# Kernel tuning notes

Measured on AMD Instinct MI355X. Metric: run time of the kernel, lower is better.

## Reference

```python
import jax, jax.numpy as jnp
import numpy as np

K_NN = 32
LN_EPS = 1e-5
P_JOINT = 0.95      # safety_priorities['structural_joints']
P_PLATFORM = 0.9    # safety_priorities['working_platforms']


def _sqdist(a, b):
    # a:[B,M,3], b:[B,N,3] -> [B,M,N] squared euclidean distances
    return jnp.maximum(jnp.sum(a * a, -1)[:, :, None] + jnp.sum(b * b, -1)[:, None, :]
                       - 2.0 * jnp.einsum('bmd,bnd->bmn', a, b), 0.0)


def _gather(arr, idx):
    # arr:[B,N,D], idx:[B,C] -> [B,C,D]
    B, C = idx.shape
    return jnp.take_along_axis(arr, jnp.broadcast_to(idx[:, :, None], (B, C, arr.shape[-1])), axis=1)


def _fps(coords, num_samples):
    # iterative farthest point sampling (deterministic start at index 0)
    B, N, _ = coords.shape
    start = jnp.zeros((B,), jnp.int32)
    dist0 = jnp.full((B, N), jnp.inf, coords.dtype)
    samp0 = jnp.zeros((B, num_samples), jnp.int32)

    def body(i, carry):
        dist, samp, last = carry
        last_pts = _gather(coords, last[:, None])                 # [B,1,3]
        d = jnp.sqrt(jnp.sum((coords - last_pts) ** 2, -1))       # [B,N]
        dist = jnp.minimum(dist, d)
        nxt = jnp.argmax(dist, 1).astype(jnp.int32)
        dist = dist.at[jnp.arange(B), nxt].set(0.0)
        samp = samp.at[:, i].set(nxt)
        return dist, samp, nxt

    _, samp, _ = jax.lax.fori_loop(1, num_samples, body, (dist0, samp0, start))
    return samp


def _safety(coords, scale):
    # per-point safety score [B,N], computed on the full point cloud (as in original)
    N = coords.shape[1]
    z = coords[:, :, 2]
    if scale == 'global':
        return 1.0 + jax.nn.sigmoid((z - z.mean(1, keepdims=True)) / 5.0) * P_JOINT
    if scale == 'component':
        zv = jnp.var(z, axis=1, keepdims=True, ddof=1)            # torch.var is unbiased
        return jnp.broadcast_to(1.0 + jnp.exp(-zv / 0.1) * P_PLATFORM, z.shape)
    # detail: full NxN cdist -> connection density (dist < 0.5  <=>  sqdist < 0.25)
    d2 = _sqdist(coords, coords)                                  # [B,N,N]
    density = jnp.sum(d2 < 0.25, -1).astype(coords.dtype)
    return 1.0 + density / N * P_JOINT


def _select_scale(features, coords, C, S, W1, b1, W2, b2, scale):
    idx = _fps(coords, C)                     # [B,C]
    cfeat = _gather(features, idx)            # [B,C,D]
    ccoord = _gather(coords, idx)             # [B,C,3]
    # kNN max-pooled local features (computed by original module; not used downstream)
    knn_d2 = _sqdist(ccoord, coords)          # [B,C,N]
    _, knn = jax.lax.top_k(-knn_d2, K_NN)
    _local = jax.vmap(lambda f, i: f[i])(features, knn).max(2)    # [B,C,D]
    # per-center safety score: per-point score gathered at FPS centers
    safety = jnp.take_along_axis(_safety(coords, scale), idx, axis=1)  # [B,C]
    # selector MLP: Linear -> ReLU -> Linear -> Sigmoid
    probs = jax.nn.sigmoid(jnp.maximum(cfeat @ W1.T + b1, 0.0) @ W2.T + b2)  # [B,C,S]
    final = probs.mean(-1) * safety           # [B,C] per-center score
    _, top = jax.lax.top_k(final, S)          # [B,S]
    return _gather(cfeat, top)                # [B,S,D]


def _forward(pf, pc, g_W1, g_b1, g_W2, g_b2, c_W1, c_b1, c_W2, c_b2,
             d_W1, d_b1, d_W2, d_b2, p_W1, p_b1, p_W2, p_b2, ln_g, ln_b):
    g = _select_scale(pf, pc, 256, 16, g_W1, g_b1, g_W2, g_b2, 'global')
    c = _select_scale(pf, pc, 128, 16, c_W1, c_b1, c_W2, c_b2, 'component')
    d = _select_scale(pf, pc, 64, 8, d_W1, d_b1, d_W2, d_b2, 'detail')
    toks = jnp.concatenate([g, c, d], 1)      # [B,40,D]
    # prompt_mlp: Linear(D,D/2) -> ReLU -> Linear(D/2,D) -> LayerNorm(D)
    h = jnp.maximum(toks @ p_W1.T + p_b1, 0.0) @ p_W2.T + p_b2
    mu = h.mean(-1, keepdims=True)
    var = h.var(-1, keepdims=True)
    return (h - mu) * jax.lax.rsqrt(var + LN_EPS) * ln_g + ln_b


def setup_inputs() -> dict:
    key = jax.random.key(0)
    B, N, D = 2, 8192, 768
    ks = iter(jax.random.split(key, 32))

    def nrm(shape, s=0.02):
        return jax.random.normal(next(ks), shape, jnp.float32) * s

    inp = {
        'point_features': jax.random.normal(next(ks), (B, N, D), jnp.float32),
        'point_coords': jax.random.normal(next(ks), (B, N, 3), jnp.float32) * 2.0,
    }
    for p, C, S in [('g', 256, 16), ('c', 128, 16), ('d', 64, 8)]:
        inp[p + '_W1'] = nrm((C, D)); inp[p + '_b1'] = jnp.zeros((C,), jnp.float32)
        inp[p + '_W2'] = nrm((S, C)); inp[p + '_b2'] = jnp.zeros((S,), jnp.float32)
    inp['p_W1'] = nrm((D // 2, D)); inp['p_b1'] = jnp.zeros((D // 2,), jnp.float32)
    inp['p_W2'] = nrm((D, D // 2)); inp['p_b2'] = jnp.zeros((D,), jnp.float32)
    inp['ln_g'] = jnp.ones((D,), jnp.float32); inp['ln_b'] = jnp.zeros((D,), jnp.float32)
    return inp


def reference(point_features, point_coords, g_W1, g_b1, g_W2, g_b2,
              c_W1, c_b1, c_W2, c_b2, d_W1, d_b1, d_W2, d_b2,
              p_W1, p_b1, p_W2, p_b2, ln_g, ln_b):
    return _forward(point_features, point_coords, g_W1, g_b1, g_W2, g_b2,
                    c_W1, c_b1, c_W2, c_b2, d_W1, d_b1, d_W2, d_b2,
                    p_W1, p_b1, p_W2, p_b2, ln_g, ln_b)
```

## Files before the change

### kernel.cpp

```cpp
#include <hip/hip_runtime.h>
#include <math.h>

#define N_PTS 8192
#define D_FEAT 768

typedef float v2f __attribute__((ext_vector_type(2)));

__device__ __forceinline__ float wred_max_f32(float x) {
    int v = __float_as_int(x), o;
    o = __builtin_amdgcn_update_dpp(0, v, 0x111, 0xf, 0xf, false); v = __float_as_int(fmaxf(__int_as_float(v), __int_as_float(o)));
    o = __builtin_amdgcn_update_dpp(0, v, 0x112, 0xf, 0xf, false); v = __float_as_int(fmaxf(__int_as_float(v), __int_as_float(o)));
    o = __builtin_amdgcn_update_dpp(0, v, 0x114, 0xf, 0xf, false); v = __float_as_int(fmaxf(__int_as_float(v), __int_as_float(o)));
    o = __builtin_amdgcn_update_dpp(0, v, 0x118, 0xf, 0xf, false); v = __float_as_int(fmaxf(__int_as_float(v), __int_as_float(o)));
    o = __builtin_amdgcn_update_dpp(0, v, 0x142, 0xa, 0xf, false); v = __float_as_int(fmaxf(__int_as_float(v), __int_as_float(o)));
    o = __builtin_amdgcn_update_dpp(0, v, 0x143, 0xc, 0xf, false); v = __float_as_int(fmaxf(__int_as_float(v), __int_as_float(o)));
    return __int_as_float(__builtin_amdgcn_readlane(v, 63));
}
__device__ __forceinline__ int wred_min_i32(int x) {
    int v = x, o;
    o = __builtin_amdgcn_update_dpp(0x7fffffff, v, 0x111, 0xf, 0xf, false); v = (o < v) ? o : v;
    o = __builtin_amdgcn_update_dpp(0x7fffffff, v, 0x112, 0xf, 0xf, false); v = (o < v) ? o : v;
    o = __builtin_amdgcn_update_dpp(0x7fffffff, v, 0x114, 0xf, 0xf, false); v = (o < v) ? o : v;
    o = __builtin_amdgcn_update_dpp(0x7fffffff, v, 0x118, 0xf, 0xf, false); v = (o < v) ? o : v;
    o = __builtin_amdgcn_update_dpp(0x7fffffff, v, 0x142, 0xa, 0xf, false); v = (o < v) ? o : v;
    o = __builtin_amdgcn_update_dpp(0x7fffffff, v, 0x143, 0xc, 0xf, false); v = (o < v) ? o : v;
    return __builtin_amdgcn_readlane(v, 63);
}
__device__ __forceinline__ float wred_add_f32(float x) {
    int v = __float_as_int(x), o;
    o = __builtin_amdgcn_update_dpp(0, v, 0x111, 0xf, 0xf, false); v = __float_as_int(__int_as_float(v) + __int_as_float(o));
    o = __builtin_amdgcn_update_dpp(0, v, 0x112, 0xf, 0xf, false); v = __float_as_int(__int_as_float(v) + __int_as_float(o));
    o = __builtin_amdgcn_update_dpp(0, v, 0x114, 0xf, 0xf, false); v = __float_as_int(__int_as_float(v) + __int_as_float(o));
    o = __builtin_amdgcn_update_dpp(0, v, 0x118, 0xf, 0xf, false); v = __float_as_int(__int_as_float(v) + __int_as_float(o));
    o = __builtin_amdgcn_update_dpp(0, v, 0x142, 0xa, 0xf, false); v = __float_as_int(__int_as_float(v) + __int_as_float(o));
    o = __builtin_amdgcn_update_dpp(0, v, 0x143, 0xc, 0xf, false); v = __float_as_int(__int_as_float(v) + __int_as_float(o));
    return __int_as_float(__builtin_amdgcn_readlane(v, 63));
}

#define DPP64_STEP(cur, ctrl, rmask)                                                        \
    {                                                                                       \
        unsigned _h = (unsigned)__builtin_amdgcn_update_dpp(0, (int)(unsigned)((cur) >> 32), ctrl, rmask, 0xf, false); \
        unsigned _l = (unsigned)__builtin_amdgcn_update_dpp(0, (int)(unsigned)(cur), ctrl, rmask, 0xf, false);         \
        unsigned long long _o = ((unsigned long long)_h << 32) | _l;                        \
        cur = (_o > (cur)) ? _o : (cur);                                                    \
    }

__global__ __launch_bounds__(512, 2) __attribute__((amdgpu_waves_per_eu(2)))
void fps_kernel(const float* __restrict__ coords,
                int* __restrict__ idx_all,
                float* __restrict__ safety_all) {
#pragma clang fp contract(off)
    const int b = blockIdx.x;
    const int t = threadIdx.x;
    const float* cb = coords + (size_t)b * N_PTS * 3;

    v2f px2[8], py2[8], pz2[8], m2p[8];
#pragma unroll
    for (int j = 0; j < 8; j++) {
        int p0 = t + (2 * j) * 512, p1 = t + (2 * j + 1) * 512;
        px2[j].x = cb[p0 * 3 + 0]; px2[j].y = cb[p1 * 3 + 0];
        py2[j].x = cb[p0 * 3 + 1]; py2[j].y = cb[p1 * 3 + 1];
        pz2[j].x = cb[p0 * 3 + 2]; pz2[j].y = cb[p1 * 3 + 2];
        m2p[j].x = INFINITY; m2p[j].y = INFINITY;
    }
    __shared__ float cbl4[N_PTS * 4];
    __shared__ unsigned long long skey[2][8];
    __shared__ int sel[256];
    __shared__ float r1s[8], r2s[8];
#pragma unroll
    for (int j = 0; j < 8; j++) {
        int p0 = t + (2 * j) * 512, p1 = t + (2 * j + 1) * 512;
        *(float4*)&cbl4[p0 * 4] = make_float4(px2[j].x, py2[j].x, pz2[j].x, 0.f);
        *(float4*)&cbl4[p1 * 4] = make_float4(px2[j].y, py2[j].y, pz2[j].y, 0.f);
    }
    if (t == 0) sel[0] = 0;
    float lx = cb[0], ly = cb[1], lz = cb[2];
    __syncthreads();

    const int lane = t & 63, w = t >> 6;
    for (int i = 1; i < 256; i++) {
        v2f Lx = {lx, lx}, Ly = {ly, ly}, Lz = {lz, lz};
#pragma unroll
        for (int j = 0; j < 8; j++) {
            v2f dx = px2[j] - Lx, dy = py2[j] - Ly, dz = pz2[j] - Lz;
            v2f d2 = dx * dx + dy * dy + dz * dz;
            m2p[j] = __builtin_elementwise_min(m2p[j], d2);
        }
        v2f q[4];
#pragma unroll
        for (int j = 0; j < 4; j++) q[j] = __builtin_elementwise_max(m2p[j], m2p[j + 4]);
        q[0] = __builtin_elementwise_max(q[0], q[2]);
        q[1] = __builtin_elementwise_max(q[1], q[3]);
        q[0] = __builtin_elementwise_max(q[0], q[1]);
        float c2 = fmaxf(q[0].x, q[0].y);
        float smax = sqrtf(c2);
        float thi = c2 * 0.9999995f;
        int tot = 0;
        int ci[8];
#pragma unroll
        for (int j = 0; j < 8; j++) {
            bool bx = (m2p[j].x >= thi);
            bool by = (m2p[j].y >= thi);
            tot += __popcll(__ballot(bx));
            tot += __popcll(__ballot(by));
            int a  = bx ? (2 * j)     : 0x7fff;
            int bb = by ? (2 * j + 1) : 0x7fff;
            ci[j] = (a < bb) ? a : bb;
        }
#pragma unroll
        for (int j = 0; j < 4; j++) ci[j] = min(ci[j], ci[j + 4]);
        int bk = min(min(ci[0], ci[1]), min(ci[2], ci[3]));
        if (tot > 64) {
            smax = -1.f; bk = 0;
#pragma unroll
            for (int k = 0; k < 16; k++) {
                float mk = (k & 1) ? m2p[k >> 1].y : m2p[k >> 1].x;
                float s = sqrtf(mk);
                if (s > smax) { smax = s; bk = k; }
            }
        }
        int bi = t + bk * 512;
        unsigned long long key = ((unsigned long long)__float_as_uint(smax) << 32)
                               | (unsigned)(0xFFFFFFFFu - (unsigned)bi);
        DPP64_STEP(key, 0x111, 0xf)
        DPP64_STEP(key, 0x112, 0xf)
        DPP64_STEP(key, 0x114, 0xf)
        DPP64_STEP(key, 0x118, 0xf)
        DPP64_STEP(key, 0x142, 0xa)
        DPP64_STEP(key, 0x143, 0xc)
        if (lane == 63) skey[i & 1][w] = key;
        __syncthreads();
        const int par = i & 1;
        unsigned long long k8 = skey[par][lane & 7];
        int cidx = (int)(0xFFFFFFFFu - (unsigned)k8);
        float spec = 0.f;
        if (lane < 24) spec = cbl4[cidx * 4 + (lane >> 3)];
        DPP64_STEP(k8, 0x111, 0xf)
        DPP64_STEP(k8, 0x112, 0xf)
        DPP64_STEP(k8, 0x114, 0xf)
        unsigned klo = (unsigned)__builtin_amdgcn_readlane((int)(unsigned)k8, 7);
        int fbi = (int)(0xFFFFFFFFu - klo);
        int ww = (fbi & 511) >> 6;
        lx = __int_as_float(__builtin_amdgcn_readlane(__float_as_int(spec), ww));
        ly = __int_as_float(__builtin_amdgcn_readlane(__float_as_int(spec), 8 + ww));
        lz = __int_as_float(__builtin_amdgcn_readlane(__float_as_int(spec), 16 + ww));
        if (t == 0) sel[i] = fbi;
    }

    __syncthreads();
    if (t < 256) {
        int v = sel[t];
        idx_all[b * 256 + t] = v;
        if (t < 128) idx_all[512 + b * 128 + t] = v;
        if (t < 64)  idx_all[768 + b * 64 + t] = v;
    }

    float s1 = 0.f, s2 = 0.f;
#pragma unroll
    for (int j = 0; j < 8; j++) {
        s1 += pz2[j].x; s2 += pz2[j].x * pz2[j].x;
        s1 += pz2[j].y; s2 += pz2[j].y * pz2[j].y;
    }
    s1 = wred_add_f32(s1);
    s2 = wred_add_f32(s2);
    if (lane == 0) { r1s[w] = s1; r2s[w] = s2; }
    __syncthreads();
    float S1 = ((r1s[0] + r1s[1]) + (r1s[2] + r1s[3])) + ((r1s[4] + r1s[5]) + (r1s[6] + r1s[7]));
    float S2 = ((r2s[0] + r2s[1]) + (r2s[2] + r2s[3])) + ((r2s[4] + r2s[5]) + (r2s[6] + r2s[7]));
    float mean = S1 / 8192.0f;
    float var1 = (S2 - S1 * S1 / 8192.0f) / 8191.0f;
    float scomp = 1.0f + expf(-var1 / 0.1f) * 0.9f;
    if (t < 256) {
        int p = sel[t];
        float z = cbl4[p * 4 + 2];
        safety_all[b * 256 + t] = 1.0f + (1.0f / (1.0f + expf(-((z - mean) / 5.0f)))) * 0.95f;
        if (t < 128) safety_all[512 + b * 128 + t] = scomp;
    }
}

#define W1_GEMM(RT)                                                            \
  {                                                                            \
    const int jg = t >> 3, rp = t & 7;                                         \
    const float* wb = W1 + (size_t)(jg * RT) * 768 + rp * 96;                  \
    float4 acc[RT][8];                                                         \
    _Pragma("unroll") for (int a = 0; a < RT; a++)                             \
      _Pragma("unroll") for (int r = 0; r < 8; r++)                            \
        acc[a][r] = make_float4(0.f, 0.f, 0.f, 0.f);                           \
    for (int s = 0; s < 96; s += 4) {                                          \
      float4 xv[8];                                                            \
      _Pragma("unroll") for (int r = 0; r < 8; r++)                            \
        xv[r] = *(const float4*)&xt[r * 772 + rp * 96 + s];                    \
      _Pragma("unroll") for (int a = 0; a < RT; a++) {                         \
        float4 wv = *(const float4*)&wb[(size_t)a * 768 + s];                  \
        _Pragma("unroll") for (int r = 0; r < 8; r++) {                        \
          acc[a][r].x = fmaf(wv.x, xv[r].x, acc[a][r].x);                      \
          acc[a][r].y = fmaf(wv.y, xv[r].y, acc[a][r].y);                      \
          acc[a][r].z = fmaf(wv.z, xv[r].z, acc[a][r].z);                      \
          acc[a][r].w = fmaf(wv.w, xv[r].w, acc[a][r].w);                      \
        }                                                                      \
      }                                                                        \
    }                                                                          \
    _Pragma("unroll") for (int a = 0; a < RT; a++)                             \
      _Pragma("unroll") for (int r = 0; r < 8; r++)                            \
        part[rp * 2048 + (jg * RT + a) * 8 + r] =                              \
            (acc[a][r].x + acc[a][r].y) + (acc[a][r].z + acc[a][r].w);         \
  }

__global__ __launch_bounds__(512) void score_kernel(
    const float* __restrict__ feat, const float* __restrict__ coords,
    const float* __restrict__ gW1, const float* __restrict__ gb1,
    const float* __restrict__ gW2, const float* __restrict__ gb2,
    const float* __restrict__ cW1, const float* __restrict__ cb1,
    const float* __restrict__ cW2, const float* __restrict__ cb2,
    const float* __restrict__ dW1, const float* __restrict__ db1,
    const float* __restrict__ dW2, const float* __restrict__ db2,
    const int* __restrict__ idx_all, const float* __restrict__ safety_all,
    float* __restrict__ final_all) {
    int bid = blockIdx.x;
    int b, c0, C, S, off;
    const float *W1, *b1, *W2, *b2;
    if (bid < 64)      { C = 256; S = 16; W1 = gW1; b1 = gb1; W2 = gW2; b2 = gb2; b = bid >> 5; c0 = (bid & 31) * 8; off = 0; }
    else if (bid < 96) { int r = bid - 64; C = 128; S = 16; W1 = cW1; b1 = cb1; W2 = cW2; b2 = cb2; b = r >> 4; c0 = (r & 15) * 8; off = 512; }
    else               { int r = bid - 96; C = 64;  S = 8;  W1 = dW1; b1 = db1; W2 = dW2; b2 = db2; b = r >> 3; c0 = (r & 7) * 8; off = 768; }
    const bool isdet = (bid >= 96);

    __shared__ float xt[8 * 772];
    __shared__ float h1s[8 * 260];
    __shared__ float part[8 * 2048];
    __shared__ float ps[8 * 16];
    __shared__ int pid[8];
    __shared__ float dpart[8][8];
    __shared__ float sdens[8];
    const int t = threadIdx.x;
    if (t < 8) pid[t] = idx_all[off + b * C + c0 + t];
    __syncthreads();

    if (isdet) {
#pragma clang fp contract(off)
        float cx[8], cy[8], cz[8], cc[8];
#pragma unroll
        for (int c = 0; c < 8; c++) {
            const float* cp = coords + ((size_t)b * N_PTS + pid[c]) * 3;
            cx[c] = cp[0]; cy[c] = cp[1]; cz[c] = cp[2];
            cc[c] = cx[c] * cx[c] + cy[c] * cy[c] + cz[c] * cz[c];
        }
        int cnt[8];
#pragma unroll
        for (int c = 0; c < 8; c++) cnt[c] = 0;
        const float* cbl = coords + (size_t)b * N_PTS * 3;
        for (int k = 0; k < 16; k++) {
            int q = t + k * 512;
            float x = cbl[q * 3], y = cbl[q * 3 + 1], z = cbl[q * 3 + 2];
            float pp = x * x + y * y + z * z;
#pragma unroll
            for (int c = 0; c < 8; c++) {
                float dot = cx[c] * x + cy[c] * y + cz[c] * z;
                float d2 = (cc[c] + pp) - 2.0f * dot;
                if (d2 < 0.25f) cnt[c]++;
            }
        }
        int wv = t >> 6;
#pragma unroll
        for (int c = 0; c < 8; c++) {
            float s = wred_add_f32((float)cnt[c]);
            if ((t & 63) == 0) dpart[wv][c] = s;
        }
    }

    for (int r = 0; r < 8; r++) {
        const float* src = feat + ((size_t)b * N_PTS + pid[r]) * D_FEAT;
        for (int c = t; c < 768; c += 512) xt[r * 772 + c] = src[c];
    }
    __syncthreads();
    if (isdet && t < 8) {
        float tot = ((dpart[0][t] + dpart[1][t]) + (dpart[2][t] + dpart[3][t]))
                  + ((dpart[4][t] + dpart[5][t]) + (dpart[6][t] + dpart[7][t]));
        sdens[t] = 1.0f + (tot / 8192.0f) * 0.95f;
    }

    if (C == 256)      W1_GEMM(4)
    else if (C == 128) W1_GEMM(2)
    else               W1_GEMM(1)
    __syncthreads();
    for (int u = t; u < C * 8; u += 512) {
        int row = u >> 3;
        float sum = ((part[u] + part[2048 + u]) + (part[4096 + u] + part[6144 + u]))
                  + ((part[8192 + u] + part[10240 + u]) + (part[12288 + u] + part[14336 + u]))
                  + b1[row];
        h1s[(u & 7) * 260 + row] = fmaxf(sum, 0.f);
    }
    __syncthreads();

    if (t < 8 * S) {
        int r = t / S, s = t % S;
        float4 a = make_float4(0, 0, 0, 0);
        for (int k = 0; k < C; k += 4) {
            float4 wv = *(const float4*)&W2[s * C + k];
            float4 h = *(const float4*)&h1s[r * 260 + k];
            a.x = fmaf(wv.x, h.x, a.x); a.y = fmaf(wv.y, h.y, a.y);
            a.z = fmaf(wv.z, h.z, a.z); a.w = fmaf(wv.w, h.w, a.w);
        }
        float logit = (a.x + a.y) + (a.z + a.w) + b2[s];
        ps[r * 16 + s] = 1.0f / (1.0f + expf(-logit));
    }
    __syncthreads();
    if (t < 8) {
        float m = 0.f;
        for (int s = 0; s < S; s++) m += ps[t * 16 + s];
        m /= (float)S;
        float saf = isdet ? sdens[t] : safety_all[off + b * C + c0 + t];
        final_all[off + b * C + c0 + t] = m * saf;
    }
}

__global__ __launch_bounds__(320) void hk_kernel(
    const float* __restrict__ feat, const int* __restrict__ idx_all,
    const float* __restrict__ final_all,
    const float* __restrict__ pW1, const float* __restrict__ pb1,
    float* __restrict__ h_buf) {
    int bid = blockIdx.x;
    int b = bid / 48, js = bid % 48;
    int t = threadIdx.x;
    __shared__ int tokp[40];
    int w = t >> 6, lane = t & 63;
    if (w < 3) {
        int sc = w;
        int C    = (sc == 0) ? 256 : (sc == 1) ? 128 : 64;
        int off  = (sc == 0) ? 0 : (sc == 1) ? 512 : 768;
        int base = (sc == 0) ? 0 : (sc == 1) ? 16 : 32;
        int S    = (sc == 2) ? 8 : 16;
        float v[4];
#pragma unroll
        for (int j = 0; j < 4; j++) {
            int ii = lane + j * 64;
            v[j] = (ii < C) ? final_all[off + b * C + ii] : -INFINITY;
        }
        for (int s = 0; s < S; s++) {
            float bd = v[0]; int bj = 0;
#pragma unroll
            for (int j = 1; j < 4; j++) if (v[j] > bd) { bd = v[j]; bj = j; }
            int bi2 = lane + bj * 64;
            float m = wred_max_f32(bd);
            int cand = (bd == m) ? bi2 : 0x7fffffff;
            int wi = wred_min_i32(cand);
            if (lane == (wi & 63)) {
#pragma unroll
                for (int j = 0; j < 4; j++) if (j == (wi >> 6)) v[j] = -INFINITY;
            }
            if (lane == 0) tokp[base + s] = idx_all[off + b * C + wi];
        }
    }
    __syncthreads();

    int tk = t % 40, jr = t / 40;
    int j = js * 8 + jr;
    int p = tokp[tk];
    const float* x = feat + ((size_t)b * N_PTS + p) * D_FEAT;
    const float* wrow = pW1 + (size_t)j * 768;
    float4 a = make_float4(0, 0, 0, 0);
    for (int k = 0; k < 768; k += 4) {
        float4 wv = *(const float4*)&wrow[k];
        float4 xv = *(const float4*)&x[k];
        a.x = fmaf(wv.x, xv.x, a.x); a.y = fmaf(wv.y, xv.y, a.y);
        a.z = fmaf(wv.z, xv.z, a.z); a.w = fmaf(wv.w, xv.w, a.w);
    }
    float v = (a.x + a.y) + (a.z + a.w) + pb1[j];
    h_buf[((size_t)b * 40 + tk) * 384 + j] = fmaxf(v, 0.f);
}

__global__ __launch_bounds__(256) void outln_kernel(
    const float* __restrict__ h_buf,
    const float* __restrict__ pW2, const float* __restrict__ pb2,
    const float* __restrict__ lng, const float* __restrict__ lnb,
    float* __restrict__ out) {
    int bid = blockIdx.x;
    int t = threadIdx.x;
    __shared__ float hs[384];
    __shared__ float red[8];
    const float* hrow = h_buf + (size_t)bid * 384;
    for (int u = t; u < 384; u += 256) hs[u] = hrow[u];
    __syncthreads();

    float vout[3];
#pragma unroll
    for (int a = 0; a < 3; a++) {
        int o = t + a * 256;
        const float* wrow = pW2 + (size_t)o * 384;
        float4 acc = make_float4(0, 0, 0, 0);
        for (int k = 0; k < 384; k += 4) {
            float4 wv = *(const float4*)&wrow[k];
            float4 hv = *(const float4*)&hs[k];
            acc.x = fmaf(wv.x, hv.x, acc.x); acc.y = fmaf(wv.y, hv.y, acc.y);
            acc.z = fmaf(wv.z, hv.z, acc.z); acc.w = fmaf(wv.w, hv.w, acc.w);
        }
        vout[a] = (acc.x + acc.y) + (acc.z + acc.w) + pb2[o];
    }

    float s1 = (vout[0] + vout[1]) + vout[2];
    float s2 = (vout[0] * vout[0] + vout[1] * vout[1]) + vout[2] * vout[2];
    s1 = wred_add_f32(s1);
    s2 = wred_add_f32(s2);
    int lane = t & 63, wid = t >> 6;
    if (lane == 0) { red[wid * 2] = s1; red[wid * 2 + 1] = s2; }
    __syncthreads();
    float S1 = (red[0] + red[2]) + (red[4] + red[6]);
    float S2 = (red[1] + red[3]) + (red[5] + red[7]);
    float mu = S1 / 768.0f;
    float var = S2 / 768.0f - mu * mu;
    float inv = rsqrtf(var + 1e-5f);
    float* dst = out + (size_t)bid * 768;
#pragma unroll
    for (int a = 0; a < 3; a++) {
        int o = t + a * 256;
        dst[o] = (vout[a] - mu) * inv * lng[o] + lnb[o];
    }
}

extern "C" void kernel_launch(void* const* d_in, const int* in_sizes, int n_in,
                              void* d_out, int out_size, void* d_ws, size_t ws_size,
                              hipStream_t stream) {
    const float* feat   = (const float*)d_in[0];
    const float* coords = (const float*)d_in[1];
    const float* gW1 = (const float*)d_in[2],  *gb1 = (const float*)d_in[3];
    const float* gW2 = (const float*)d_in[4],  *gb2 = (const float*)d_in[5];
    const float* cW1 = (const float*)d_in[6],  *cb1 = (const float*)d_in[7];
    const float* cW2 = (const float*)d_in[8],  *cb2 = (const float*)d_in[9];
    const float* dW1 = (const float*)d_in[10], *db1 = (const float*)d_in[11];
    const float* dW2 = (const float*)d_in[12], *db2 = (const float*)d_in[13];
    const float* pW1 = (const float*)d_in[14], *pb1 = (const float*)d_in[15];
    const float* pW2 = (const float*)d_in[16], *pb2 = (const float*)d_in[17];
    const float* lng = (const float*)d_in[18], *lnb = (const float*)d_in[19];
    float* out = (float*)d_out;

    int*   idx_all    = (int*)d_ws;
    float* safety_all = (float*)d_ws + 896;
    float* final_all  = (float*)d_ws + 1792;
    float* h_buf      = (float*)d_ws + 2688;

    fps_kernel<<<2, 512, 0, stream>>>(coords, idx_all, safety_all);
    score_kernel<<<112, 512, 0, stream>>>(feat, coords, gW1, gb1, gW2, gb2, cW1, cb1, cW2, cb2,
                                          dW1, db1, dW2, db2, idx_all, safety_all, final_all);
    hk_kernel<<<96, 320, 0, stream>>>(feat, idx_all, final_all, pW1, pb1, h_buf);
    outln_kernel<<<80, 256, 0, stream>>>(h_buf, pW2, pb2, lng, lnb, out);
}
```

Baseline: 532.8 us.

## Fuse four kernels into one cooperative kernel with grid-wide syncs

Replaces the separate FPS, scoring, head-projection and output-LayerNorm launches with a single cooperative mega-kernel of 112 blocks that separates the phases with grid.sync() and reuses one shared-memory buffer. The aim is to remove the launch overhead and inter-kernel gaps between four dependent launches. In exchange, the scoring phase is capped at 512 threads per block under 2-waves-per-EU register limits, later phases run with idle blocks, and grid barriers add their own cost. The FPS phase still runs on only two blocks while the other 110 wait at the first barrier.

After: 634.4 us. +19.1%, slower.

```diff
diff --git a/kernel.cpp b/kernel.cpp
--- a/kernel.cpp
+++ b/kernel.cpp
@@ -1,5 +1,8 @@
 #include <hip/hip_runtime.h>
+#include <hip/hip_cooperative_groups.h>
 #include <math.h>
+
+namespace cg = cooperative_groups;
 
 #define N_PTS 8192
 #define D_FEAT 768
@@ -45,139 +48,6 @@
         cur = (_o > (cur)) ? _o : (cur);                                                    \
     }
 
-__global__ __launch_bounds__(512, 2) __attribute__((amdgpu_waves_per_eu(2)))
-void fps_kernel(const float* __restrict__ coords,
-                int* __restrict__ idx_all,
-                float* __restrict__ safety_all) {
-#pragma clang fp contract(off)
-    const int b = blockIdx.x;
-    const int t = threadIdx.x;
-    const float* cb = coords + (size_t)b * N_PTS * 3;
-
-    v2f px2[8], py2[8], pz2[8], m2p[8];
-#pragma unroll
-    for (int j = 0; j < 8; j++) {
-        int p0 = t + (2 * j) * 512, p1 = t + (2 * j + 1) * 512;
-        px2[j].x = cb[p0 * 3 + 0]; px2[j].y = cb[p1 * 3 + 0];
-        py2[j].x = cb[p0 * 3 + 1]; py2[j].y = cb[p1 * 3 + 1];
-        pz2[j].x = cb[p0 * 3 + 2]; pz2[j].y = cb[p1 * 3 + 2];
-        m2p[j].x = INFINITY; m2p[j].y = INFINITY;
-    }
-    __shared__ float cbl4[N_PTS * 4];
-    __shared__ unsigned long long skey[2][8];
-    __shared__ int sel[256];
-    __shared__ float r1s[8], r2s[8];
-#pragma unroll
-    for (int j = 0; j < 8; j++) {
-        int p0 = t + (2 * j) * 512, p1 = t + (2 * j + 1) * 512;
-        *(float4*)&cbl4[p0 * 4] = make_float4(px2[j].x, py2[j].x, pz2[j].x, 0.f);
-        *(float4*)&cbl4[p1 * 4] = make_float4(px2[j].y, py2[j].y, pz2[j].y, 0.f);
-    }
-    if (t == 0) sel[0] = 0;
-    float lx = cb[0], ly = cb[1], lz = cb[2];
-    __syncthreads();
-
-    const int lane = t & 63, w = t >> 6;
-    for (int i = 1; i < 256; i++) {
-        v2f Lx = {lx, lx}, Ly = {ly, ly}, Lz = {lz, lz};
-#pragma unroll
-        for (int j = 0; j < 8; j++) {
-            v2f dx = px2[j] - Lx, dy = py2[j] - Ly, dz = pz2[j] - Lz;
-            v2f d2 = dx * dx + dy * dy + dz * dz;
-            m2p[j] = __builtin_elementwise_min(m2p[j], d2);
-        }
-        v2f q[4];
-#pragma unroll
-        for (int j = 0; j < 4; j++) q[j] = __builtin_elementwise_max(m2p[j], m2p[j + 4]);
-        q[0] = __builtin_elementwise_max(q[0], q[2]);
-        q[1] = __builtin_elementwise_max(q[1], q[3]);
-        q[0] = __builtin_elementwise_max(q[0], q[1]);
-        float c2 = fmaxf(q[0].x, q[0].y);
-        float smax = sqrtf(c2);
-        float thi = c2 * 0.9999995f;
-        int tot = 0;
-        int ci[8];
-#pragma unroll
-        for (int j = 0; j < 8; j++) {
-            bool bx = (m2p[j].x >= thi);
-            bool by = (m2p[j].y >= thi);
-            tot += __popcll(__ballot(bx));
-            tot += __popcll(__ballot(by));
-            int a  = bx ? (2 * j)     : 0x7fff;
-            int bb = by ? (2 * j + 1) : 0x7fff;
-            ci[j] = (a < bb) ? a : bb;
-        }
-#pragma unroll
-        for (int j = 0; j < 4; j++) ci[j] = min(ci[j], ci[j + 4]);
-        int bk = min(min(ci[0], ci[1]), min(ci[2], ci[3]));
-        if (tot > 64) {
-            smax = -1.f; bk = 0;
-#pragma unroll
-            for (int k = 0; k < 16; k++) {
-                float mk = (k & 1) ? m2p[k >> 1].y : m2p[k >> 1].x;
-                float s = sqrtf(mk);
-                if (s > smax) { smax = s; bk = k; }
-            }
-        }
-        int bi = t + bk * 512;
-        unsigned long long key = ((unsigned long long)__float_as_uint(smax) << 32)
-                               | (unsigned)(0xFFFFFFFFu - (unsigned)bi);
-        DPP64_STEP(key, 0x111, 0xf)
-        DPP64_STEP(key, 0x112, 0xf)
-        DPP64_STEP(key, 0x114, 0xf)
-        DPP64_STEP(key, 0x118, 0xf)
-        DPP64_STEP(key, 0x142, 0xa)
-        DPP64_STEP(key, 0x143, 0xc)
-        if (lane == 63) skey[i & 1][w] = key;
-        __syncthreads();
-        const int par = i & 1;
-        unsigned long long k8 = skey[par][lane & 7];
-        int cidx = (int)(0xFFFFFFFFu - (unsigned)k8);
-        float spec = 0.f;
-        if (lane < 24) spec = cbl4[cidx * 4 + (lane >> 3)];
-        DPP64_STEP(k8, 0x111, 0xf)
-        DPP64_STEP(k8, 0x112, 0xf)
-        DPP64_STEP(k8, 0x114, 0xf)
-        unsigned klo = (unsigned)__builtin_amdgcn_readlane((int)(unsigned)k8, 7);
-        int fbi = (int)(0xFFFFFFFFu - klo);
-        int ww = (fbi & 511) >> 6;
-        lx = __int_as_float(__builtin_amdgcn_readlane(__float_as_int(spec), ww));
-        ly = __int_as_float(__builtin_amdgcn_readlane(__float_as_int(spec), 8 + ww));
-        lz = __int_as_float(__builtin_amdgcn_readlane(__float_as_int(spec), 16 + ww));
-        if (t == 0) sel[i] = fbi;
-    }
-
-    __syncthreads();
-    if (t < 256) {
-        int v = sel[t];
-        idx_all[b * 256 + t] = v;
-        if (t < 128) idx_all[512 + b * 128 + t] = v;
-        if (t < 64)  idx_all[768 + b * 64 + t] = v;
-    }
-
-    float s1 = 0.f, s2 = 0.f;
-#pragma unroll
-    for (int j = 0; j < 8; j++) {
-        s1 += pz2[j].x; s2 += pz2[j].x * pz2[j].x;
-        s1 += pz2[j].y; s2 += pz2[j].y * pz2[j].y;
-    }
-    s1 = wred_add_f32(s1);
-    s2 = wred_add_f32(s2);
-    if (lane == 0) { r1s[w] = s1; r2s[w] = s2; }
-    __syncthreads();
-    float S1 = ((r1s[0] + r1s[1]) + (r1s[2] + r1s[3])) + ((r1s[4] + r1s[5]) + (r1s[6] + r1s[7]));
-    float S2 = ((r2s[0] + r2s[1]) + (r2s[2] + r2s[3])) + ((r2s[4] + r2s[5]) + (r2s[6] + r2s[7]));
-    float mean = S1 / 8192.0f;
-    float var1 = (S2 - S1 * S1 / 8192.0f) / 8191.0f;
-    float scomp = 1.0f + expf(-var1 / 0.1f) * 0.9f;
-    if (t < 256) {
-        int p = sel[t];
-        float z = cbl4[p * 4 + 2];
-        safety_all[b * 256 + t] = 1.0f + (1.0f / (1.0f + expf(-((z - mean) / 5.0f)))) * 0.95f;
-        if (t < 128) safety_all[512 + b * 128 + t] = scomp;
-    }
-}
-
 #define W1_GEMM(RT)                                                            \
   {                                                                            \
     const int jg = t >> 3, rp = t & 7;                                         \
@@ -206,213 +76,344 @@
             (acc[a][r].x + acc[a][r].y) + (acc[a][r].z + acc[a][r].w);         \
   }
 
-__global__ __launch_bounds__(512) void score_kernel(
-    const float* __restrict__ feat, const float* __restrict__ coords,
-    const float* __restrict__ gW1, const float* __restrict__ gb1,
-    const float* __restrict__ gW2, const float* __restrict__ gb2,
-    const float* __restrict__ cW1, const float* __restrict__ cb1,
-    const float* __restrict__ cW2, const float* __restrict__ cb2,
-    const float* __restrict__ dW1, const float* __restrict__ db1,
-    const float* __restrict__ dW2, const float* __restrict__ db2,
-    const int* __restrict__ idx_all, const float* __restrict__ safety_all,
-    float* __restrict__ final_all) {
-    int bid = blockIdx.x;
-    int b, c0, C, S, off;
-    const float *W1, *b1, *W2, *b2;
-    if (bid < 64)      { C = 256; S = 16; W1 = gW1; b1 = gb1; W2 = gW2; b2 = gb2; b = bid >> 5; c0 = (bid & 31) * 8; off = 0; }
-    else if (bid < 96) { int r = bid - 64; C = 128; S = 16; W1 = cW1; b1 = cb1; W2 = cW2; b2 = cb2; b = r >> 4; c0 = (r & 15) * 8; off = 512; }
-    else               { int r = bid - 96; C = 64;  S = 8;  W1 = dW1; b1 = db1; W2 = dW2; b2 = db2; b = r >> 3; c0 = (r & 7) * 8; off = 768; }
-    const bool isdet = (bid >= 96);
-
-    __shared__ float xt[8 * 772];
-    __shared__ float h1s[8 * 260];
-    __shared__ float part[8 * 2048];
-    __shared__ float ps[8 * 16];
-    __shared__ int pid[8];
-    __shared__ float dpart[8][8];
-    __shared__ float sdens[8];
+__global__ __launch_bounds__(512, 2) __attribute__((amdgpu_waves_per_eu(2)))
+void mega_kernel(const float* __restrict__ feat, const float* __restrict__ coords,
+                 const float* __restrict__ gW1, const float* __restrict__ gb1,
+                 const float* __restrict__ gW2, const float* __restrict__ gb2,
+                 const float* __restrict__ cW1, const float* __restrict__ cb1,
+                 const float* __restrict__ cW2, const float* __restrict__ cb2,
+                 const float* __restrict__ dW1, const float* __restrict__ db1,
+                 const float* __restrict__ dW2, const float* __restrict__ db2,
+                 const float* __restrict__ pW1, const float* __restrict__ pb1,
+                 const float* __restrict__ pW2, const float* __restrict__ pb2,
+                 const float* __restrict__ lng, const float* __restrict__ lnb,
+                 float* __restrict__ out,
+                 int* __restrict__ idx_all, float* __restrict__ safety_all,
+                 float* __restrict__ final_all, float* __restrict__ h_buf) {
+    cg::grid_group grid = cg::this_grid();
+    __shared__ __align__(16) float smem[33280];
+    const int bid = blockIdx.x;
     const int t = threadIdx.x;
-    if (t < 8) pid[t] = idx_all[off + b * C + c0 + t];
-    __syncthreads();
-
-    if (isdet) {
+    const int lane = t & 63, w = t >> 6;
+
+    if (bid < 2) {
 #pragma clang fp contract(off)
-        float cx[8], cy[8], cz[8], cc[8];
-#pragma unroll
-        for (int c = 0; c < 8; c++) {
-            const float* cp = coords + ((size_t)b * N_PTS + pid[c]) * 3;
-            cx[c] = cp[0]; cy[c] = cp[1]; cz[c] = cp[2];
-            cc[c] = cx[c] * cx[c] + cy[c] * cy[c] + cz[c] * cz[c];
-        }
-        int cnt[8];
-#pragma unroll
-        for (int c = 0; c < 8; c++) cnt[c] = 0;
-        const float* cbl = coords + (size_t)b * N_PTS * 3;
-        for (int k = 0; k < 16; k++) {
-            int q = t + k * 512;
-            float x = cbl[q * 3], y = cbl[q * 3 + 1], z = cbl[q * 3 + 2];
-            float pp = x * x + y * y + z * z;
+        const int b = bid;
+        const float* cb = coords + (size_t)b * N_PTS * 3;
+        float* cbl4 = smem;
+        unsigned long long* skey = (unsigned long long*)(smem + 32768);
+        int* sel = (int*)(smem + 32800);
+        float* r1s = smem + 33056, *r2s = smem + 33064;
+
+        v2f px2[8], py2[8], pz2[8], m2p[8];
+#pragma unroll
+        for (int j = 0; j < 8; j++) {
+            int p0 = t + (2 * j) * 512, p1 = t + (2 * j + 1) * 512;
+            px2[j].x = cb[p0 * 3 + 0]; px2[j].y = cb[p1 * 3 + 0];
+            py2[j].x = cb[p0 * 3 + 1]; py2[j].y = cb[p1 * 3 + 1];
+            pz2[j].x = cb[p0 * 3 + 2]; pz2[j].y = cb[p1 * 3 + 2];
+            m2p[j].x = INFINITY; m2p[j].y = INFINITY;
+        }
+#pragma unroll
+        for (int j = 0; j < 8; j++) {
+            int p0 = t + (2 * j) * 512, p1 = t + (2 * j + 1) * 512;
+            *(float4*)&cbl4[p0 * 4] = make_float4(px2[j].x, py2[j].x, pz2[j].x, 0.f);
+            *(float4*)&cbl4[p1 * 4] = make_float4(px2[j].y, py2[j].y, pz2[j].y, 0.f);
+        }
+        if (t == 0) sel[0] = 0;
+        float lx = cb[0], ly = cb[1], lz = cb[2];
+        __syncthreads();
+
+        for (int i = 1; i < 256; i++) {
+            v2f Lx = {lx, lx}, Ly = {ly, ly}, Lz = {lz, lz};
+#pragma unroll
+            for (int j = 0; j < 8; j++) {
+                v2f dx = px2[j] - Lx, dy = py2[j] - Ly, dz = pz2[j] - Lz;
+                v2f d2 = dx * dx + dy * dy + dz * dz;
+                m2p[j] = __builtin_elementwise_min(m2p[j], d2);
+            }
+            v2f q[4];
+#pragma unroll
+            for (int j = 0; j < 4; j++) q[j] = __builtin_elementwise_max(m2p[j], m2p[j + 4]);
+            q[0] = __builtin_elementwise_max(q[0], q[2]);
+            q[1] = __builtin_elementwise_max(q[1], q[3]);
+            q[0] = __builtin_elementwise_max(q[0], q[1]);
+            float c2 = fmaxf(q[0].x, q[0].y);
+            float smax = sqrtf(c2);
+            float thi = c2 * 0.9999995f;
+            int tot = 0;
+            int ci[8];
+#pragma unroll
+            for (int j = 0; j < 8; j++) {
+                bool bx = (m2p[j].x >= thi);
+                bool by = (m2p[j].y >= thi);
+                tot += __popcll(__ballot(bx));
+                tot += __popcll(__ballot(by));
+                int a  = bx ? (2 * j)     : 0x7fff;
+                int bb = by ? (2 * j + 1) : 0x7fff;
+                ci[j] = (a < bb) ? a : bb;
+            }
+#pragma unroll
+            for (int j = 0; j < 4; j++) ci[j] = min(ci[j], ci[j + 4]);
+            int bk = min(min(ci[0], ci[1]), min(ci[2], ci[3]));
+            if (tot > 64) {
+                smax = -1.f; bk = 0;
+#pragma unroll
+                for (int k = 0; k < 16; k++) {
+                    float mk = (k & 1) ? m2p[k >> 1].y : m2p[k >> 1].x;
+                    float s = sqrtf(mk);
+                    if (s > smax) { smax = s; bk = k; }
+                }
+            }
+            int bi = t + bk * 512;
+            unsigned long long key = ((unsigned long long)__float_as_uint(smax) << 32)
+                                   | (unsigned)(0xFFFFFFFFu - (unsigned)bi);
+            DPP64_STEP(key, 0x111, 0xf)
+            DPP64_STEP(key, 0x112, 0xf)
+            DPP64_STEP(key, 0x114, 0xf)
+            DPP64_STEP(key, 0x118, 0xf)
+            DPP64_STEP(key, 0x142, 0xa)
+            DPP64_STEP(key, 0x143, 0xc)
+            if (lane == 63) skey[(i & 1) * 8 + w] = key;
+            __syncthreads();
+            const int par = i & 1;
+            unsigned long long k8 = skey[par * 8 + (lane & 7)];
+            int cidx = (int)(0xFFFFFFFFu - (unsigned)k8);
+            float spec = 0.f;
+            if (lane < 24) spec = cbl4[cidx * 4 + (lane >> 3)];
+            DPP64_STEP(k8, 0x111, 0xf)
+            DPP64_STEP(k8, 0x112, 0xf)
+            DPP64_STEP(k8, 0x114, 0xf)
+            unsigned klo = (unsigned)__builtin_amdgcn_readlane((int)(unsigned)k8, 7);
+            int fbi = (int)(0xFFFFFFFFu - klo);
+            int ww = (fbi & 511) >> 6;
+            lx = __int_as_float(__builtin_amdgcn_readlane(__float_as_int(spec), ww));
+            ly = __int_as_float(__builtin_amdgcn_readlane(__float_as_int(spec), 8 + ww));
+            lz = __int_as_float(__builtin_amdgcn_readlane(__float_as_int(spec), 16 + ww));
+            if (t == 0) sel[i] = fbi;
+        }
+
+        __syncthreads();
+        if (t < 256) {
+            int v = sel[t];
+            idx_all[b * 256 + t] = v;
+            if (t < 128) idx_all[512 + b * 128 + t] = v;
+            if (t < 64)  idx_all[768 + b * 64 + t] = v;
+        }
+        float s1 = 0.f, s2 = 0.f;
+#pragma unroll
+        for (int j = 0; j < 8; j++) {
+            s1 += pz2[j].x; s2 += pz2[j].x * pz2[j].x;
+            s1 += pz2[j].y; s2 += pz2[j].y * pz2[j].y;
+        }
+        s1 = wred_add_f32(s1);
+        s2 = wred_add_f32(s2);
+        if (lane == 0) { r1s[w] = s1; r2s[w] = s2; }
+        __syncthreads();
+        float S1 = ((r1s[0] + r1s[1]) + (r1s[2] + r1s[3])) + ((r1s[4] + r1s[5]) + (r1s[6] + r1s[7]));
+        float S2 = ((r2s[0] + r2s[1]) + (r2s[2] + r2s[3])) + ((r2s[4] + r2s[5]) + (r2s[6] + r2s[7]));
+        float mean = S1 / 8192.0f;
+        float var1 = (S2 - S1 * S1 / 8192.0f) / 8191.0f;
+        float scomp = 1.0f + expf(-var1 / 0.1f) * 0.9f;
+        if (t < 256) {
+            int p = sel[t];
+            float z = cbl4[p * 4 + 2];
+            safety_all[b * 256 + t] = 1.0f + (1.0f / (1.0f + expf(-((z - mean) / 5.0f)))) * 0.95f;
+            if (t < 128) safety_all[512 + b * 128 + t] = scomp;
+        }
+    }
+    grid.sync();
+
+    {
+        int b, c0, C, S, off;
+        const float *W1, *b1, *W2, *b2;
+        if (bid < 64)      { C = 256; S = 16; W1 = gW1; b1 = gb1; W2 = gW2; b2 = gb2; b = bid >> 5; c0 = (bid & 31) * 8; off = 0; }
+        else if (bid < 96) { int r = bid - 64; C = 128; S = 16; W1 = cW1; b1 = cb1; W2 = cW2; b2 = cb2; b = r >> 4; c0 = (r & 15) * 8; off = 512; }
+        else               { int r = bid - 96; C = 64;  S = 8;  W1 = dW1; b1 = db1; W2 = dW2; b2 = db2; b = r >> 3; c0 = (r & 7) * 8; off = 768; }
+        const bool isdet = (bid >= 96);
+
+        float* xt   = smem;
+        float* h1s  = smem + 6176;
+        float* part = smem + 8256;
+        float* ps   = smem + 24640;
+        int*   pid  = (int*)(smem + 24768);
+        float* dpart= smem + 24776;
+        float* sdens= smem + 24840;
+
+        if (t < 8) pid[t] = idx_all[off + b * C + c0 + t];
+        __syncthreads();
+
+        if (isdet) {
+#pragma clang fp contract(off)
+            float cx[8], cy[8], cz[8], cc[8];
 #pragma unroll
             for (int c = 0; c < 8; c++) {
-                float dot = cx[c] * x + cy[c] * y + cz[c] * z;
-                float d2 = (cc[c] + pp) - 2.0f * dot;
-                if (d2 < 0.25f) cnt[c]++;
-            }
-        }
-        int wv = t >> 6;
-#pragma unroll
-        for (int c = 0; c < 8; c++) {
-            float s = wred_add_f32((float)cnt[c]);
-            if ((t & 63) == 0) dpart[wv][c] = s;
+                const float* cp = coords + ((size_t)b * N_PTS + pid[c]) * 3;
+                cx[c] = cp[0]; cy[c] = cp[1]; cz[c] = cp[2];
+                cc[c] = cx[c] * cx[c] + cy[c] * cy[c] + cz[c] * cz[c];
+            }
+            int cnt[8];
+#pragma unroll
+            for (int c = 0; c < 8; c++) cnt[c] = 0;
+            const float* cbl = coords + (size_t)b * N_PTS * 3;
+            for (int k = 0; k < 16; k++) {
+                int q = t + k * 512;
+                float x = cbl[q * 3], y = cbl[q * 3 + 1], z = cbl[q * 3 + 2];
+                float pp = x * x + y * y + z * z;
+#pragma unroll
+                for (int c = 0; c < 8; c++) {
+                    float dot = cx[c] * x + cy[c] * y + cz[c] * z;
+                    float d2 = (cc[c] + pp) - 2.0f * dot;
+                    if (d2 < 0.25f) cnt[c]++;
+                }
+            }
+#pragma unroll
+            for (int c = 0; c < 8; c++) {
+                float s = wred_add_f32((float)cnt[c]);
+                if (lane == 0) dpart[w * 8 + c] = s;
+            }
+        }
+
+        for (int r = 0; r < 8; r++) {
+            const float* src = feat + ((size_t)b * N_PTS + pid[r]) * D_FEAT;
+            for (int c = t; c < 768; c += 512) xt[r * 772 + c] = src[c];
+        }
+        __syncthreads();
+        if (isdet && t < 8) {
+            float tot = ((dpart[0 + t] + dpart[8 + t]) + (dpart[16 + t] + dpart[24 + t]))
+                      + ((dpart[32 + t] + dpart[40 + t]) + (dpart[48 + t] + dpart[56 + t]));
+            sdens[t] = 1.0f + (tot / 8192.0f) * 0.95f;
+        }
+
+        if (C == 256)      W1_GEMM(4)
+        else if (C == 128) W1_GEMM(2)
+        else               W1_GEMM(1)
+        __syncthreads();
+        for (int u = t; u < C * 8; u += 512) {
+            int row = u >> 3;
+            float sum = ((part[u] + part[2048 + u]) + (part[4096 + u] + part[6144 + u]))
+                      + ((part[8192 + u] + part[10240 + u]) + (part[12288 + u] + part[14336 + u]))
+                      + b1[row];
+            h1s[(u & 7) * 260 + row] = fmaxf(sum, 0.f);
+        }
+        __syncthreads();
+
+        if (t < 8 * S) {
+            int r = t / S, s = t % S;
+            float4 a = make_float4(0, 0, 0, 0);
+            for (int k = 0; k < C; k += 4) {
+                float4 wv = *(const float4*)&W2[s * C + k];
+                float4 h = *(const float4*)&h1s[r * 260 + k];
+                a.x = fmaf(wv.x, h.x, a.x); a.y = fmaf(wv.y, h.y, a.y);
+                a.z = fmaf(wv.z, h.z, a.z); a.w = fmaf(wv.w, h.w, a.w);
+            }
+            float logit = (a.x + a.y) + (a.z + a.w) + b2[s];
+            ps[r * 16 + s] = 1.0f / (1.0f + expf(-logit));
+        }
+        __syncthreads();
+        if (t < 8) {
+            float m = 0.f;
+            for (int s = 0; s < S; s++) m += ps[t * 16 + s];
+            m /= (float)S;
+            float saf = isdet ? sdens[t] : safety_all[off + b * C + c0 + t];
+            final_all[off + b * C + c0 + t] = m * saf;
         }
     }
-
-    for (int r = 0; r < 8; r++) {
-        const float* src = feat + ((size_t)b * N_PTS + pid[r]) * D_FEAT;
-        for (int c = t; c < 768; c += 512) xt[r * 772 + c] = src[c];
+    grid.sync();
+
+    if (bid < 96) {
+        int b = bid / 48, js = bid % 48;
+        int* tokp = (int*)smem;
+        if (w < 3) {
+            int sc = w;
+            int C    = (sc == 0) ? 256 : (sc == 1) ? 128 : 64;
+            int off  = (sc == 0) ? 0 : (sc == 1) ? 512 : 768;
+            int base = (sc == 0) ? 0 : (sc == 1) ? 16 : 32;
+            int S    = (sc == 2) ? 8 : 16;
+            float v[4];
+#pragma unroll
+            for (int j = 0; j < 4; j++) {
+                int ii = lane + j * 64;
+                v[j] = (ii < C) ? final_all[off + b * C + ii] : -INFINITY;
+            }
+            for (int s = 0; s < S; s++) {
+                float bd = v[0]; int bj = 0;
+#pragma unroll
+                for (int j = 1; j < 4; j++) if (v[j] > bd) { bd = v[j]; bj = j; }
+                int bi2 = lane + bj * 64;
+                float m = wred_max_f32(bd);
+                int cand = (bd == m) ? bi2 : 0x7fffffff;
+                int wi = wred_min_i32(cand);
+                if (lane == (wi & 63)) {
+#pragma unroll
+                    for (int j = 0; j < 4; j++) if (j == (wi >> 6)) v[j] = -INFINITY;
+                }
+                if (lane == 0) tokp[base + s] = idx_all[off + b * C + wi];
+            }
+        }
+        __syncthreads();
+
+        if (t < 320) {
+            int tk = t % 40, jr = t / 40;
+            int j = js * 8 + jr;
+            int p = tokp[tk];
+            const float* x = feat + ((size_t)b * N_PTS + p) * D_FEAT;
+            const float* wrow = pW1 + (size_t)j * 768;
+            float4 a = make_float4(0, 0, 0, 0);
+            for (int k = 0; k < 768; k += 4) {
+                float4 wv = *(const float4*)&wrow[k];
+                float4 xv = *(const float4*)&x[k];
+                a.x = fmaf(wv.x, xv.x, a.x); a.y = fmaf(wv.y, xv.y, a.y);
+                a.z = fmaf(wv.z, xv.z, a.z); a.w = fmaf(wv.w, xv.w, a.w);
+            }
+            float v = (a.x + a.y) + (a.z + a.w) + pb1[j];
+            h_buf[((size_t)b * 40 + tk) * 384 + j] = fmaxf(v, 0.f);
+        }
     }
-    __syncthreads();
-    if (isdet && t < 8) {
-        float tot = ((dpart[0][t] + dpart[1][t]) + (dpart[2][t] + dpart[3][t]))
-                  + ((dpart[4][t] + dpart[5][t]) + (dpart[6][t] + dpart[7][t]));
-        sdens[t] = 1.0f + (tot / 8192.0f) * 0.95f;
-    }
-
-    if (C == 256)      W1_GEMM(4)
-    else if (C == 128) W1_GEMM(2)
-    else               W1_GEMM(1)
-    __syncthreads();
-    for (int u = t; u < C * 8; u += 512) {
-        int row = u >> 3;
-        float sum = ((part[u] + part[2048 + u]) + (part[4096 + u] + part[6144 + u]))
-                  + ((part[8192 + u] + part[10240 + u]) + (part[12288 + u] + part[14336 + u]))
-                  + b1[row];
-        h1s[(u & 7) * 260 + row] = fmaxf(sum, 0.f);
-    }
-    __syncthreads();
-
-    if (t < 8 * S) {
-        int r = t / S, s = t % S;
-        float4 a = make_float4(0, 0, 0, 0);
-        for (int k = 0; k < C; k += 4) {
-            float4 wv = *(const float4*)&W2[s * C + k];
-            float4 h = *(const float4*)&h1s[r * 260 + k];
-            a.x = fmaf(wv.x, h.x, a.x); a.y = fmaf(wv.y, h.y, a.y);
-            a.z = fmaf(wv.z, h.z, a.z); a.w = fmaf(wv.w, h.w, a.w);
-        }
-        float logit = (a.x + a.y) + (a.z + a.w) + b2[s];
-        ps[r * 16 + s] = 1.0f / (1.0f + expf(-logit));
-    }
-    __syncthreads();
-    if (t < 8) {
-        float m = 0.f;
-        for (int s = 0; s < S; s++) m += ps[t * 16 + s];
-        m /= (float)S;
-        float saf = isdet ? sdens[t] : safety_all[off + b * C + c0 + t];
-        final_all[off + b * C + c0 + t] = m * saf;
-    }
-}
-
-__global__ __launch_bounds__(320) void hk_kernel(
-    const float* __restrict__ feat, const int* __restrict__ idx_all,
-    const float* __restrict__ final_all,
-    const float* __restrict__ pW1, const float* __restrict__ pb1,
-    float* __restrict__ h_buf) {
-    int bid = blockIdx.x;
-    int b = bid / 48, js = bid % 48;
-    int t = threadIdx.x;
-    __shared__ int tokp[40];
-    int w = t >> 6, lane = t & 63;
-    if (w < 3) {
-        int sc = w;
-        int C    = (sc == 0) ? 256 : (sc == 1) ? 128 : 64;
-        int off  = (sc == 0) ? 0 : (sc == 1) ? 512 : 768;
-        int base = (sc == 0) ? 0 : (sc == 1) ? 16 : 32;
-        int S    = (sc == 2) ? 8 : 16;
-        float v[4];
-#pragma unroll
-        for (int j = 0; j < 4; j++) {
-            int ii = lane + j * 64;
-            v[j] = (ii < C) ? final_all[off + b * C + ii] : -INFINITY;
-        }
-        for (int s = 0; s < S; s++) {
-            float bd = v[0]; int bj = 0;
-#pragma unroll
-            for (int j = 1; j < 4; j++) if (v[j] > bd) { bd = v[j]; bj = j; }
-            int bi2 = lane + bj * 64;
-            float m = wred_max_f32(bd);
-            int cand = (bd == m) ? bi2 : 0x7fffffff;
-            int wi = wred_min_i32(cand);
-            if (lane == (wi & 63)) {
-#pragma unroll
-                for (int j = 0; j < 4; j++) if (j == (wi >> 6)) v[j] = -INFINITY;
-            }
-            if (lane == 0) tokp[base + s] = idx_all[off + b * C + wi];
-        }
-    }
-    __syncthreads();
-
-    int tk = t % 40, jr = t / 40;
-    int j = js * 8 + jr;
-    int p = tokp[tk];
-    const float* x = feat + ((size_t)b * N_PTS + p) * D_FEAT;
-    const float* wrow = pW1 + (size_t)j * 768;
-    float4 a = make_float4(0, 0, 0, 0);
-    for (int k = 0; k < 768; k += 4) {
-        float4 wv = *(const float4*)&wrow[k];
-        float4 xv = *(const float4*)&x[k];
-        a.x = fmaf(wv.x, xv.x, a.x); a.y = fmaf(wv.y, xv.y, a.y);
-        a.z = fmaf(wv.z, xv.z, a.z); a.w = fmaf(wv.w, xv.w, a.w);
-    }
-    float v = (a.x + a.y) + (a.z + a.w) + pb1[j];
-    h_buf[((size_t)b * 40 + tk) * 384 + j] = fmaxf(v, 0.f);
-}
-
-__global__ __launch_bounds__(256) void outln_kernel(
-    const float* __restrict__ h_buf,
-    const float* __restrict__ pW2, const float* __restrict__ pb2,
-    const float* __restrict__ lng, const float* __restrict__ lnb,
-    float* __restrict__ out) {
-    int bid = blockIdx.x;
-    int t = threadIdx.x;
-    __shared__ float hs[384];
-    __shared__ float red[8];
-    const float* hrow = h_buf + (size_t)bid * 384;
-    for (int u = t; u < 384; u += 256) hs[u] = hrow[u];
-    __syncthreads();
-
-    float vout[3];
-#pragma unroll
-    for (int a = 0; a < 3; a++) {
-        int o = t + a * 256;
-        const float* wrow = pW2 + (size_t)o * 384;
-        float4 acc = make_float4(0, 0, 0, 0);
-        for (int k = 0; k < 384; k += 4) {
-            float4 wv = *(const float4*)&wrow[k];
-            float4 hv = *(const float4*)&hs[k];
-            acc.x = fmaf(wv.x, hv.x, acc.x); acc.y = fmaf(wv.y, hv.y, acc.y);
-            acc.z = fmaf(wv.z, hv.z, acc.z); acc.w = fmaf(wv.w, hv.w, acc.w);
-        }
-        vout[a] = (acc.x + acc.y) + (acc.z + acc.w) + pb2[o];
-    }
-
-    float s1 = (vout[0] + vout[1]) + vout[2];
-    float s2 = (vout[0] * vout[0] + vout[1] * vout[1]) + vout[2] * vout[2];
-    s1 = wred_add_f32(s1);
-    s2 = wred_add_f32(s2);
-    int lane = t & 63, wid = t >> 6;
-    if (lane == 0) { red[wid * 2] = s1; red[wid * 2 + 1] = s2; }
-    __syncthreads();
-    float S1 = (red[0] + red[2]) + (red[4] + red[6]);
-    float S2 = (red[1] + red[3]) + (red[5] + red[7]);
-    float mu = S1 / 768.0f;
-    float var = S2 / 768.0f - mu * mu;
-    float inv = rsqrtf(var + 1e-5f);
-    float* dst = out + (size_t)bid * 768;
-#pragma unroll
-    for (int a = 0; a < 3; a++) {
-        int o = t + a * 256;
-        dst[o] = (vout[a] - mu) * inv * lng[o] + lnb[o];
+    grid.sync();
+
+    if (bid < 80) {
+        float* hs = smem;
+        float* red = smem + 384;
+        const float* hrow = h_buf + (size_t)bid * 384;
+        for (int u = t; u < 384; u += 512) hs[u] = hrow[u];
+        __syncthreads();
+
+        float vout[3];
+        if (t < 256) {
+#pragma unroll
+            for (int a = 0; a < 3; a++) {
+                int o = t + a * 256;
+                const float* wrow = pW2 + (size_t)o * 384;
+                float4 acc = make_float4(0, 0, 0, 0);
+                for (int k = 0; k < 384; k += 4) {
+                    float4 wv = *(const float4*)&wrow[k];
+                    float4 hv = *(const float4*)&hs[k];
+                    acc.x = fmaf(wv.x, hv.x, acc.x); acc.y = fmaf(wv.y, hv.y, acc.y);
+                    acc.z = fmaf(wv.z, hv.z, acc.z); acc.w = fmaf(wv.w, hv.w, acc.w);
+                }
+                vout[a] = (acc.x + acc.y) + (acc.z + acc.w) + pb2[o];
+            }
+            float s1 = (vout[0] + vout[1]) + vout[2];
+            float s2 = (vout[0] * vout[0] + vout[1] * vout[1]) + vout[2] * vout[2];
+            s1 = wred_add_f32(s1);
+            s2 = wred_add_f32(s2);
+            if (lane == 0) { red[w * 2] = s1; red[w * 2 + 1] = s2; }
+        }
+        __syncthreads();
+        if (t < 256) {
+            float S1 = (red[0] + red[2]) + (red[4] + red[6]);
+            float S2 = (red[1] + red[3]) + (red[5] + red[7]);
+            float mu = S1 / 768.0f;
+            float var = S2 / 768.0f - mu * mu;
+            float inv = rsqrtf(var + 1e-5f);
+            float* dst = out + (size_t)bid * 768;
+#pragma unroll
+            for (int a = 0; a < 3; a++) {
+                int o = t + a * 256;
+                dst[o] = (vout[a] - mu) * inv * lng[o] + lnb[o];
+            }
+        }
     }
 }
 
@@ -437,9 +438,8 @@
     float* final_all  = (float*)d_ws + 1792;
     float* h_buf      = (float*)d_ws + 2688;
 
-    fps_kernel<<<2, 512, 0, stream>>>(coords, idx_all, safety_all);
-    score_kernel<<<112, 512, 0, stream>>>(feat, coords, gW1, gb1, gW2, gb2, cW1, cb1, cW2, cb2,
-                                          dW1, db1, dW2, db2, idx_all, safety_all, final_all);
-    hk_kernel<<<96, 320, 0, stream>>>(feat, idx_all, final_all, pW1, pb1, h_buf);
-    outln_kernel<<<80, 256, 0, stream>>>(h_buf, pW2, pb2, lng, lnb, out);
+    void* args[] = {&feat, &coords, &gW1, &gb1, &gW2, &gb2, &cW1, &cb1, &cW2, &cb2,
+                    &dW1, &db1, &dW2, &db2, &pW1, &pb1, &pW2, &pb2, &lng, &lnb,
+                    &out, &idx_all, &safety_all, &final_all, &h_buf};
+    hipLaunchCooperativeKernel((void*)mega_kernel, dim3(112), dim3(512), args, 0, stream);
 }
```
